# Performance work log

Measured on AMD Instinct MI355X. Metric: run time of the kernel, lower is better.

Reference implementation:

```python
import math
import jax, jax.numpy as jnp
import numpy as np

B, T, G, E, H, L = 8, 32, 32, 768, 12, 4
S = T * G
HD = E // H


def setup_inputs() -> dict:
    key = jax.random.key(0)
    ks = jax.random.split(key, 10)
    def n(k, shape, s=0.02):
        return s * jax.random.normal(k, shape, jnp.float32)
    return dict(
        x=jax.random.normal(ks[0], (B, T, G, E), jnp.float32),
        study_date=jnp.sort(jax.random.randint(ks[1], (B, T), 0, 50), axis=-1),
        wpe=n(ks[2], (50, E)),
        ln1_w=jnp.ones((L, E)), ln1_b=jnp.zeros((L, E)),
        in_w=n(ks[3], (L, 3 * E, E)), in_b=jnp.zeros((L, 3 * E)),
        out_w=n(ks[4], (L, E, E)), out_b=jnp.zeros((L, E)),
        ln2_w=jnp.ones((L, E)), ln2_b=jnp.zeros((L, E)),
        fc_w=n(ks[5], (L, 4 * E, E)), fc_b=jnp.zeros((L, 4 * E)),
        proj_w=n(ks[6], (L, E, 4 * E), 0.02 / math.sqrt(2 * L)),
        proj_b=jnp.zeros((L, E)),
        lnf_w=jnp.ones((E,)), lnf_b=jnp.zeros((E,)),
    )


def _ln(x, w, b):
    m = x.mean(-1, keepdims=True)
    v = ((x - m) ** 2).mean(-1, keepdims=True)
    return (x - m) / jnp.sqrt(v + 1e-5) * w + b


def _gelu_new(x):
    # NewGELU: 0.5*x*(1+tanh(sqrt(2/pi)*(x+0.044715*x^3)))
    c = np.sqrt(2.0 / np.pi).astype(np.float32)
    return 0.5 * x * (1.0 + jnp.tanh(c * (x + 0.044715 * x ** 3)))


def _mask_bias():
    # block-causal mask: tril over T blocks, each expanded to G x G
    allowed = jnp.tril(jnp.ones((T, T), bool))
    allowed = jnp.repeat(jnp.repeat(allowed, G, axis=0), G, axis=1)  # [S,S]
    return jnp.where(allowed, 0.0, -jnp.inf).astype(jnp.float32)


def reference(x, study_date, wpe, ln1_w, ln1_b, in_w, in_b, out_w, out_b,
              ln2_w, ln2_b, fc_w, fc_b, proj_w, proj_b, lnf_w, lnf_b):
    b, t, g, d = x.shape
    s = t * g
    pos = wpe[jnp.clip(study_date, 0, 49)]  # [B,T,E]
    pos = jnp.broadcast_to(pos[:, :, None, :], (b, t, g, d)).reshape(b, s, d)
    h = x.reshape(b, s, d) + pos
    bias = _mask_bias()  # [S,S]
    inv_sqrt_hd = 1.0 / np.sqrt(HD).astype(np.float32)
    for l in range(L):
        y = _ln(h, ln1_w[l], ln1_b[l])
        qkv = y @ in_w[l].T + in_b[l]  # [B,S,3E]
        q, k, v = jnp.split(qkv, 3, axis=-1)
        q = q.reshape(b, s, H, HD).transpose(0, 2, 1, 3)
        k = k.reshape(b, s, H, HD).transpose(0, 2, 1, 3)
        v = v.reshape(b, s, H, HD).transpose(0, 2, 1, 3)
        att = jnp.einsum('bhqd,bhkd->bhqk', q, k) * inv_sqrt_hd + bias
        att = jax.nn.softmax(att, axis=-1)
        o = jnp.einsum('bhqk,bhkd->bhqd', att, v)
        o = o.transpose(0, 2, 1, 3).reshape(b, s, d)
        h = h + o @ out_w[l].T + out_b[l]
        y2 = _ln(h, ln2_w[l], ln2_b[l])
        h = h + _gelu_new(y2 @ fc_w[l].T + fc_b[l]) @ proj_w[l].T + proj_b[l]
    return _ln(h, lnf_w, lnf_b)
```

## Files before the change

kernel.cpp:

```cpp
#include <hip/hip_runtime.h>
#include <hip/hip_bf16.h>

typedef __attribute__((ext_vector_type(8))) __bf16 bf16x8;
typedef __attribute__((ext_vector_type(4))) float f32x4;

typedef unsigned short u16;

__device__ __forceinline__ u16 f2bf(float f) {
    unsigned int u = __float_as_uint(f);
    u += 0x7FFFu + ((u >> 16) & 1u);
    return (u16)(u >> 16);
}

__device__ __forceinline__ void g2l16(const void* g, void* l) {
    __builtin_amdgcn_global_load_lds(
        (const __attribute__((address_space(1))) void*)g,
        (__attribute__((address_space(3))) void*)l, 16, 0, 0);
}

#define BB 8
#define SS 1024
#define EE 768
#define HH 12
#define HD 64
#define LL 4

__global__ __launch_bounds__(256) void cvt_k(const float* __restrict__ in,
                                             u16* __restrict__ out, int n4) {
    for (int i = blockIdx.x * 256 + threadIdx.x; i < n4; i += gridDim.x * 256) {
        float4 v = ((const float4*)in)[i];
        ushort4 u;
        u.x = f2bf(v.x); u.y = f2bf(v.y); u.z = f2bf(v.z); u.w = f2bf(v.w);
        ((ushort4*)out)[i] = u;
    }
}

__global__ __launch_bounds__(256) void embed_k(const float* __restrict__ x,
                                               const int* __restrict__ sd,
                                               const float* __restrict__ wpe,
                                               float* __restrict__ h) {
    int idx = blockIdx.x * 256 + threadIdx.x;
    int e4 = idx % 192;
    int bs = idx / 192;
    int b = bs >> 10;
    int t = (bs >> 5) & 31;
    int date = sd[b * 32 + t];
    date = date < 0 ? 0 : (date > 49 ? 49 : date);
    float4 xv = ((const float4*)x)[idx];
    float4 pv = ((const float4*)wpe)[date * 192 + e4];
    float4 r; r.x = xv.x + pv.x; r.y = xv.y + pv.y; r.z = xv.z + pv.z; r.w = xv.w + pv.w;
    ((float4*)h)[idx] = r;
}

template <bool BF16OUT>
__global__ __launch_bounds__(256) void ln_k(const float* __restrict__ in,
                                            const float* __restrict__ w,
                                            const float* __restrict__ b,
                                            void* __restrict__ out) {
    int tid = threadIdx.x, wv = tid >> 6, lane = tid & 63;
    int token = blockIdx.x * 4 + wv;
    const float4* ip = (const float4*)(in + (size_t)token * EE);
    float4 v[3];
#pragma unroll
    for (int p = 0; p < 3; p++) v[p] = ip[p * 64 + lane];
    float s = 0.f;
#pragma unroll
    for (int p = 0; p < 3; p++) s += v[p].x + v[p].y + v[p].z + v[p].w;
#pragma unroll
    for (int m = 1; m < 64; m <<= 1) s += __shfl_xor(s, m);
    float mean = s * (1.f / 768.f);
    float vs = 0.f;
#pragma unroll
    for (int p = 0; p < 3; p++) {
        float dx = v[p].x - mean, dy = v[p].y - mean, dz = v[p].z - mean, dw = v[p].w - mean;
        vs += dx * dx + dy * dy + dz * dz + dw * dw;
    }
#pragma unroll
    for (int m = 1; m < 64; m <<= 1) vs += __shfl_xor(vs, m);
    float rstd = rsqrtf(vs * (1.f / 768.f) + 1e-5f);
    const float4* wp = (const float4*)w;
    const float4* bp = (const float4*)b;
#pragma unroll
    for (int p = 0; p < 3; p++) {
        float4 wv4 = wp[p * 64 + lane], bv4 = bp[p * 64 + lane];
        float rx = (v[p].x - mean) * rstd * wv4.x + bv4.x;
        float ry = (v[p].y - mean) * rstd * wv4.y + bv4.y;
        float rz = (v[p].z - mean) * rstd * wv4.z + bv4.z;
        float rw = (v[p].w - mean) * rstd * wv4.w + bv4.w;
        if (BF16OUT) {
            ushort4 u; u.x = f2bf(rx); u.y = f2bf(ry); u.z = f2bf(rz); u.w = f2bf(rw);
            ((ushort4*)((u16*)out + (size_t)token * EE))[p * 64 + lane] = u;
        } else {
            float4 r; r.x = rx; r.y = ry; r.z = rz; r.w = rw;
            ((float4*)((float*)out + (size_t)token * EE))[p * 64 + lane] = r;
        }
    }
}

template <int MODE, int BM>
__global__ __launch_bounds__(256) void gemm_bt(const u16* __restrict__ A,
                                               const u16* __restrict__ Bw,
                                               const float* __restrict__ bias,
                                               float* __restrict__ hres,
                                               u16* __restrict__ outb,
                                               u16* __restrict__ vT,
                                               u16* __restrict__ kT,
                                               int M, int N, int K) {
    constexpr int TM = BM / 32;
    constexpr int ABUF = BM * 32;
    __shared__ u16 As[2][ABUF];
    __shared__ u16 Bs[2][4096];
    const int tid = threadIdx.x;
    const int lane = tid & 63, w = tid >> 6;
    const int quad = lane >> 4, l16 = lane & 15;

    const int nx = N >> 7;
    const int ny = M / BM;
    const int id = blockIdx.x;
    const int xcd = id & 7, s = id >> 3;
    const int yt = xcd * (ny >> 3) + s / nx;
    const int xt = s % nx;
    const int m0 = yt * BM, n0 = xt * 128;
    const int wm = (w >> 1) * (BM / 2), wn = (w & 1) * 64;

    f32x4 acc[TM][4];
#pragma unroll
    for (int i = 0; i < TM; i++)
#pragma unroll
        for (int j = 0; j < 4; j++) acc[i][j] = (f32x4){0.f, 0.f, 0.f, 0.f};

    const int cB0 = w * 128 + lane, cB1 = cB0 + 64;
    const int rB0 = cB0 >> 2, gB0 = (((cB0 & 3) ^ ((cB0 >> 3) & 3)) * 8);
    const int rB1 = cB1 >> 2, gB1 = (((cB1 & 3) ^ ((cB1 >> 3) & 3)) * 8);
    const u16* Bp0 = Bw + (size_t)(n0 + rB0) * K + gB0;
    const u16* Bp1 = Bw + (size_t)(n0 + rB1) * K + gB1;
    char* lB0 = (char*)Bs + w * 2048;
    char* lB1 = (char*)Bs + w * 2048 + 1024;
    const int cA0 = (BM == 128) ? cB0 : (w * 64 + lane);
    const int rA0 = cA0 >> 2, gA0 = (((cA0 & 3) ^ ((cA0 >> 3) & 3)) * 8);
    const u16* Ap0 = A + (size_t)(m0 + rA0) * K + gA0;
    char* lA0 = (char*)As + ((BM == 128) ? w * 2048 : w * 1024);
    const int cA1 = cB1;
    const int rA1 = cA1 >> 2, gA1 = (((cA1 & 3) ^ ((cA1 >> 3) & 3)) * 8);
    const u16* Ap1 = A + (size_t)(m0 + rA1) * K + gA1;
    char* lA1 = (char*)As + w * 2048 + 1024;

    const int swz = (quad ^ ((l16 >> 1) & 3)) * 8;

    const int nk = K >> 5;
    g2l16(Ap0, lA0);
    if (BM == 128) g2l16(Ap1, lA1);
    g2l16(Bp0, lB0); g2l16(Bp1, lB1);

    for (int ki = 0; ki < nk; ki++) {
        __syncthreads();
        if (ki + 1 < nk) {
            const int kb = (ki + 1) << 5;
            const int boA = ((ki + 1) & 1) * (ABUF * 2);
            const int boB = ((ki + 1) & 1) * 8192;
            g2l16(Ap0 + kb, lA0 + boA);
            if (BM == 128) g2l16(Ap1 + kb, lA1 + boA);
            g2l16(Bp0 + kb, lB0 + boB);
            g2l16(Bp1 + kb, lB1 + boB);
        }
        const u16* Ab = (const u16*)As + (ki & 1) * ABUF;
        const u16* Bb = (const u16*)Bs + (ki & 1) * 4096;
        bf16x8 af[TM], bfr[4];
#pragma unroll
        for (int t = 0; t < TM; t++) {
            int rowA = wm + t * 16 + l16;
            af[t] = *(const bf16x8*)(Ab + rowA * 32 + swz);
        }
#pragma unroll
        for (int t = 0; t < 4; t++) {
            int rowB = wn + t * 16 + l16;
            bfr[t] = *(const bf16x8*)(Bb + rowB * 32 + swz);
        }
#pragma unroll
        for (int tm = 0; tm < TM; tm++)
#pragma unroll
            for (int tn = 0; tn < 4; tn++)
                acc[tm][tn] = __builtin_amdgcn_mfma_f32_16x16x32_bf16(
                    af[tm], bfr[tn], acc[tm][tn], 0, 0, 0);
    }

#pragma unroll
    for (int tm = 0; tm < TM; tm++) {
        int rowm = m0 + wm + tm * 16 + quad * 4;
#pragma unroll
        for (int tn = 0; tn < 4; tn++) {
            int coln = n0 + wn + tn * 16 + l16;
            float bv = bias[coln];
            f32x4 v = acc[tm][tn];
            if (MODE == 0) {
                int b = rowm >> 10, s2 = rowm & 1023;
                if (coln < EE) {
                    int hh = coln >> 6, d = coln & 63;
                    u16* qp = outb + ((size_t)(b * HH + hh) * SS + s2) * HD + d;
#pragma unroll
                    for (int r = 0; r < 4; r++) qp[r * HD] = f2bf(v[r] + bv);
                } else if (coln < 2 * EE) {
                    int hh = (coln - EE) >> 6, d = (coln - EE) & 63;
                    u16* kp = kT + ((size_t)(b * HH + hh) * SS + s2) * HD + d;
#pragma unroll
                    for (int r = 0; r < 4; r++) kp[r * HD] = f2bf(v[r] + bv);
                } else {
                    int hh = (coln - 2 * EE) >> 6, d = (coln - 2 * EE) & 63;
                    ushort4 pk;
                    pk.x = f2bf(v[0] + bv); pk.y = f2bf(v[1] + bv);
                    pk.z = f2bf(v[2] + bv); pk.w = f2bf(v[3] + bv);
                    *(ushort4*)(vT + (((size_t)((b * HH + hh) * HD + d)) << 10) + s2) = pk;
                }
            } else if (MODE == 1) {
#pragma unroll
                for (int r = 0; r < 4; r++) {
                    size_t idx = (size_t)(rowm + r) * N + coln;
                    hres[idx] += v[r] + bv;
                }
            } else {
#pragma unroll
                for (int r = 0; r < 4; r++) {
                    float x = v[r] + bv;
                    float t = x + 0.044715f * x * x * x;
                    float e = __expf(-1.5957691216057308f * t);
                    float th = (1.f - e) / (1.f + e);
                    outb[(size_t)(rowm + r) * N + coln] = f2bf(0.5f * x * (1.f + th));
                }
            }
        }
    }
}

__global__ __launch_bounds__(256) void attn_k(const u16* __restrict__ qT,
                                              const u16* __restrict__ kT,
                                              const u16* __restrict__ vT,
                                              u16* __restrict__ o) {
    __shared__ u16 Ks[2048];
    __shared__ u16 Vs[2048];
    __shared__ u16 P[4][16 * 40];
    int tid = threadIdx.x, w = tid >> 6, lane = tid & 63;
    int quad = lane >> 4, l16 = lane & 15;
    int blk = blockIdx.x;
    int qg = 15 - (blk / 96);
    int bh = blk % 96;
    int b = bh / HH, hh = bh % HH;
    int q0 = qg * 64;
    int kend_blk = q0 + 64;
    int kend_w = q0 + ((w >> 1) ? 64 : 32);

    const u16* qbase = qT + ((size_t)bh * SS + q0 + w * 16 + l16) * HD + quad * 8;
    bf16x8 qf0 = *(const bf16x8*)(qbase);
    bf16x8 qf1 = *(const bf16x8*)(qbase + 32);

    f32x4 of[4];
#pragma unroll
    for (int i = 0; i < 4; i++) of[i] = (f32x4){0.f, 0.f, 0.f, 0.f};
    float mrun[4], lrun[4];
#pragma unroll
    for (int r = 0; r < 4; r++) { mrun[r] = -__builtin_inff(); lrun[r] = 0.f; }

    int tK = tid >> 3, dcK = ((tid & 7) ^ (tK & 7));
    const u16* kg = kT + ((size_t)bh * SS + tK) * HD + dcK * 8;
    char* kl = (char*)Ks + w * 1024;
    int dV = tid >> 2, tcV = ((tid & 3) ^ ((dV >> 1) & 3));
    const u16* vg = vT + ((size_t)bh * HD + dV) * SS + tcV * 8;
    char* vl = (char*)Vs + w * 1024;
    u16* Pw = P[w];

    for (int kb = 0; kb < kend_blk; kb += 32) {
        g2l16(kg + (size_t)kb * HD, kl);
        g2l16(vg + kb, vl);
        __syncthreads();
        if (kb < kend_w) {
            int t0 = l16, t1 = 16 + l16;
            bf16x8 k00 = *(const bf16x8*)(Ks + (t0 * 8 + (quad ^ (l16 & 7))) * 8);
            bf16x8 k01 = *(const bf16x8*)(Ks + (t0 * 8 + ((4 + quad) ^ (l16 & 7))) * 8);
            bf16x8 k10 = *(const bf16x8*)(Ks + (t1 * 8 + (quad ^ (l16 & 7))) * 8);
            bf16x8 k11 = *(const bf16x8*)(Ks + (t1 * 8 + ((4 + quad) ^ (l16 & 7))) * 8);
            f32x4 s0 = (f32x4){0.f, 0.f, 0.f, 0.f};
            f32x4 s1 = (f32x4){0.f, 0.f, 0.f, 0.f};
            s0 = __builtin_amdgcn_mfma_f32_16x16x32_bf16(qf0, k00, s0, 0, 0, 0);
            s0 = __builtin_amdgcn_mfma_f32_16x16x32_bf16(qf1, k01, s0, 0, 0, 0);
            s1 = __builtin_amdgcn_mfma_f32_16x16x32_bf16(qf0, k10, s1, 0, 0, 0);
            s1 = __builtin_amdgcn_mfma_f32_16x16x32_bf16(qf1, k11, s1, 0, 0, 0);

            float alpha[4];
#pragma unroll
            for (int r = 0; r < 4; r++) {
                float a0 = s0[r] * 0.125f, a1 = s1[r] * 0.125f;
                float mx = fmaxf(a0, a1);
#pragma unroll
                for (int m = 1; m < 16; m <<= 1) mx = fmaxf(mx, __shfl_xor(mx, m));
                float mnew = fmaxf(mrun[r], mx);
                alpha[r] = __expf(mrun[r] - mnew);
                float p0 = __expf(a0 - mnew);
                float p1 = __expf(a1 - mnew);
                float ps = p0 + p1;
#pragma unroll
                for (int m = 1; m < 16; m <<= 1) ps += __shfl_xor(ps, m);
                lrun[r] = lrun[r] * alpha[r] + ps;
                mrun[r] = mnew;
                Pw[(quad * 4 + r) * 40 + l16] = f2bf(p0);
                Pw[(quad * 4 + r) * 40 + 16 + l16] = f2bf(p1);
            }
#pragma unroll
            for (int n4 = 0; n4 < 4; n4++) {
                of[n4][0] *= alpha[0]; of[n4][1] *= alpha[1];
                of[n4][2] *= alpha[2]; of[n4][3] *= alpha[3];
            }
            bf16x8 pf = *(const bf16x8*)(Pw + l16 * 40 + quad * 8);
#pragma unroll
            for (int n4 = 0; n4 < 4; n4++) {
                int d = n4 * 16 + l16;
                bf16x8 vf = *(const bf16x8*)(Vs + (d * 4 + (quad ^ ((d >> 1) & 3))) * 8);
                of[n4] = __builtin_amdgcn_mfma_f32_16x16x32_bf16(pf, vf, of[n4], 0, 0, 0);
            }
        }
        __syncthreads();
    }

    float inv[4];
#pragma unroll
    for (int r = 0; r < 4; r++) inv[r] = 1.f / lrun[r];
#pragma unroll
    for (int n4 = 0; n4 < 4; n4++)
#pragma unroll
        for (int r = 0; r < 4; r++)
            o[(size_t)(b * SS + q0 + w * 16 + quad * 4 + r) * EE + hh * HD + n4 * 16 + l16] =
                f2bf(of[n4][r] * inv[r]);
}

extern "C" void kernel_launch(void* const* d_in, const int* in_sizes, int n_in,
                              void* d_out, int out_size, void* d_ws, size_t ws_size,
                              hipStream_t stream) {
    const float* x     = (const float*)d_in[0];
    const int*   sd    = (const int*)d_in[1];
    const float* wpe   = (const float*)d_in[2];
    const float* ln1w  = (const float*)d_in[3];
    const float* ln1b  = (const float*)d_in[4];
    const float* in_w  = (const float*)d_in[5];
    const float* in_b  = (const float*)d_in[6];
    const float* out_w = (const float*)d_in[7];
    const float* out_b = (const float*)d_in[8];
    const float* ln2w  = (const float*)d_in[9];
    const float* ln2b  = (const float*)d_in[10];
    const float* fc_w  = (const float*)d_in[11];
    const float* fc_b  = (const float*)d_in[12];
    const float* pr_w  = (const float*)d_in[13];
    const float* pr_b  = (const float*)d_in[14];
    const float* lnfw  = (const float*)d_in[15];
    const float* lnfb  = (const float*)d_in[16];
    float* outp = (float*)d_out;

    char* ws = (char*)d_ws;
    float* h   = (float*)ws;
    u16* ybuf  = (u16*)(ws + 25165824);
    u16* big   = (u16*)(ws + 37748736);
    u16* qT    = big;
    u16* kT    = big + 6291456;
    u16* vT    = (u16*)(ws + 88080384);
    u16* wb    = (u16*)(ws + 100663296);
    u16* w_in  = wb;
    u16* w_out = w_in + 7077888;
    u16* w_fc  = w_out + 2359296;
    u16* w_pr  = w_fc + 9437184;

    cvt_k<<<1024, 256, 0, stream>>>(in_w,  w_in,  7077888 / 4);
    cvt_k<<<1024, 256, 0, stream>>>(out_w, w_out, 2359296 / 4);
    cvt_k<<<1024, 256, 0, stream>>>(fc_w,  w_fc,  9437184 / 4);
    cvt_k<<<1024, 256, 0, stream>>>(pr_w,  w_pr,  9437184 / 4);
    embed_k<<<6144, 256, 0, stream>>>(x, sd, wpe, h);

    for (int l = 0; l < LL; l++) {
        ln_k<true><<<2048, 256, 0, stream>>>(h, ln1w + l * EE, ln1b + l * EE, ybuf);
        gemm_bt<0, 128><<<18 * 64, 256, 0, stream>>>(
            ybuf, w_in + (size_t)l * 2304 * 768, in_b + l * 2304, nullptr, qT, vT, kT,
            8192, 2304, 768);
        attn_k<<<1536, 256, 0, stream>>>(qT, kT, vT, ybuf);
        gemm_bt<1, 64><<<6 * 128, 256, 0, stream>>>(
            ybuf, w_out + (size_t)l * 768 * 768, out_b + l * 768, h, nullptr, nullptr, nullptr,
            8192, 768, 768);
        ln_k<true><<<2048, 256, 0, stream>>>(h, ln2w + l * EE, ln2b + l * EE, ybuf);
        gemm_bt<2, 128><<<24 * 64, 256, 0, stream>>>(
            ybuf, w_fc + (size_t)l * 3072 * 768, fc_b + l * 3072, nullptr, big, nullptr, nullptr,
            8192, 3072, 768);
        gemm_bt<1, 64><<<6 * 128, 256, 0, stream>>>(
            big, w_pr + (size_t)l * 768 * 3072, pr_b + l * 768, h, nullptr, nullptr, nullptr,
            8192, 768, 3072);
    }
    ln_k<false><<<2048, 256, 0, stream>>>(h, lnfw, lnfb, outp);
}
```

Measured before the change: 1.343 ms.

## Use 4-stage LDS ring with prefetch distance 2 for BM=64 GEMM

For the BM=64 GEMM variant, the double-buffered LDS staging is replaced with a four-slot ring buffer that prefetches two K-steps ahead. Explicit vmcnt waits plus a bare s_barrier stand in for __syncthreads, so loads stay in flight across iterations. The BM=128 path is left functionally unchanged. This trades more LDS per block (48KB) for deeper latency hiding, which may reduce occupancy, and it depends on hand-coded waitcnt encodings being correct.

Result: no change. 1.332 ms (-0.9%).

```diff
diff --git a/kernel.cpp b/kernel.cpp
--- a/kernel.cpp
+++ b/kernel.cpp
@@ -107,9 +107,6 @@
                                                u16* __restrict__ kT,
                                                int M, int N, int K) {
     constexpr int TM = BM / 32;
-    constexpr int ABUF = BM * 32;
-    __shared__ u16 As[2][ABUF];
-    __shared__ u16 Bs[2][4096];
     const int tid = threadIdx.x;
     const int lane = tid & 63, w = tid >> 6;
     const int quad = lane >> 4, l16 = lane & 15;
@@ -129,59 +126,102 @@
 #pragma unroll
         for (int j = 0; j < 4; j++) acc[i][j] = (f32x4){0.f, 0.f, 0.f, 0.f};
 
-    const int cB0 = w * 128 + lane, cB1 = cB0 + 64;
-    const int rB0 = cB0 >> 2, gB0 = (((cB0 & 3) ^ ((cB0 >> 3) & 3)) * 8);
-    const int rB1 = cB1 >> 2, gB1 = (((cB1 & 3) ^ ((cB1 >> 3) & 3)) * 8);
-    const u16* Bp0 = Bw + (size_t)(n0 + rB0) * K + gB0;
-    const u16* Bp1 = Bw + (size_t)(n0 + rB1) * K + gB1;
-    char* lB0 = (char*)Bs + w * 2048;
-    char* lB1 = (char*)Bs + w * 2048 + 1024;
-    const int cA0 = (BM == 128) ? cB0 : (w * 64 + lane);
-    const int rA0 = cA0 >> 2, gA0 = (((cA0 & 3) ^ ((cA0 >> 3) & 3)) * 8);
-    const u16* Ap0 = A + (size_t)(m0 + rA0) * K + gA0;
-    char* lA0 = (char*)As + ((BM == 128) ? w * 2048 : w * 1024);
-    const int cA1 = cB1;
-    const int rA1 = cA1 >> 2, gA1 = (((cA1 & 3) ^ ((cA1 >> 3) & 3)) * 8);
-    const u16* Ap1 = A + (size_t)(m0 + rA1) * K + gA1;
-    char* lA1 = (char*)As + w * 2048 + 1024;
-
     const int swz = (quad ^ ((l16 >> 1) & 3)) * 8;
-
     const int nk = K >> 5;
-    g2l16(Ap0, lA0);
-    if (BM == 128) g2l16(Ap1, lA1);
-    g2l16(Bp0, lB0); g2l16(Bp1, lB1);
-
-    for (int ki = 0; ki < nk; ki++) {
-        __syncthreads();
-        if (ki + 1 < nk) {
-            const int kb = (ki + 1) << 5;
-            const int boA = ((ki + 1) & 1) * (ABUF * 2);
-            const int boB = ((ki + 1) & 1) * 8192;
-            g2l16(Ap0 + kb, lA0 + boA);
-            if (BM == 128) g2l16(Ap1 + kb, lA1 + boA);
-            g2l16(Bp0 + kb, lB0 + boB);
-            g2l16(Bp1 + kb, lB1 + boB);
+
+    if constexpr (BM == 128) {
+        __shared__ u16 As[2][4096];
+        __shared__ u16 Bs[2][4096];
+        const int c0 = w * 128 + lane, c1 = c0 + 64;
+        const int r0 = c0 >> 2, g0 = (((c0 & 3) ^ ((c0 >> 3) & 3)) * 8);
+        const int r1 = c1 >> 2, g1 = (((c1 & 3) ^ ((c1 >> 3) & 3)) * 8);
+        const u16* Ap0 = A + (size_t)(m0 + r0) * K + g0;
+        const u16* Ap1 = A + (size_t)(m0 + r1) * K + g1;
+        const u16* Bp0 = Bw + (size_t)(n0 + r0) * K + g0;
+        const u16* Bp1 = Bw + (size_t)(n0 + r1) * K + g1;
+        char* lA0 = (char*)As + w * 2048;
+        char* lA1 = (char*)As + w * 2048 + 1024;
+        char* lB0 = (char*)Bs + w * 2048;
+        char* lB1 = (char*)Bs + w * 2048 + 1024;
+
+        g2l16(Ap0, lA0); g2l16(Ap1, lA1); g2l16(Bp0, lB0); g2l16(Bp1, lB1);
+
+        for (int ki = 0; ki < nk; ki++) {
+            __syncthreads();
+            if (ki + 1 < nk) {
+                const int kb = (ki + 1) << 5;
+                const int bo = ((ki + 1) & 1) * 8192;
+                g2l16(Ap0 + kb, lA0 + bo);
+                g2l16(Ap1 + kb, lA1 + bo);
+                g2l16(Bp0 + kb, lB0 + bo);
+                g2l16(Bp1 + kb, lB1 + bo);
+            }
+            const u16* Ab = (const u16*)As + (ki & 1) * 4096;
+            const u16* Bb = (const u16*)Bs + (ki & 1) * 4096;
+            bf16x8 af[TM], bfr[4];
+#pragma unroll
+            for (int t = 0; t < TM; t++)
+                af[t] = *(const bf16x8*)(Ab + (wm + t * 16 + l16) * 32 + swz);
+#pragma unroll
+            for (int t = 0; t < 4; t++)
+                bfr[t] = *(const bf16x8*)(Bb + (wn + t * 16 + l16) * 32 + swz);
+#pragma unroll
+            for (int tm = 0; tm < TM; tm++)
+#pragma unroll
+                for (int tn = 0; tn < 4; tn++)
+                    acc[tm][tn] = __builtin_amdgcn_mfma_f32_16x16x32_bf16(
+                        af[tm], bfr[tn], acc[tm][tn], 0, 0, 0);
         }
-        const u16* Ab = (const u16*)As + (ki & 1) * ABUF;
-        const u16* Bb = (const u16*)Bs + (ki & 1) * 4096;
-        bf16x8 af[TM], bfr[4];
-#pragma unroll
-        for (int t = 0; t < TM; t++) {
-            int rowA = wm + t * 16 + l16;
-            af[t] = *(const bf16x8*)(Ab + rowA * 32 + swz);
+    } else {
+        __shared__ u16 SM[4 * 6144];
+        const int cA = tid;
+        const int rA = cA >> 2, gA = (((cA & 3) ^ ((cA >> 3) & 3)) * 8);
+        const u16* Ap = A + (size_t)(m0 + rA) * K + gA;
+        const int cB0 = w * 128 + lane, cB1 = cB0 + 64;
+        const int rB0 = cB0 >> 2, gB0 = (((cB0 & 3) ^ ((cB0 >> 3) & 3)) * 8);
+        const int rB1 = cB1 >> 2, gB1 = (((cB1 & 3) ^ ((cB1 >> 3) & 3)) * 8);
+        const u16* Bp0 = Bw + (size_t)(n0 + rB0) * K + gB0;
+        const u16* Bp1 = Bw + (size_t)(n0 + rB1) * K + gB1;
+        char* lA = (char*)SM + w * 1024;
+        char* lB0 = (char*)SM + 4096 + w * 2048;
+        char* lB1 = (char*)SM + 4096 + w * 2048 + 1024;
+
+        g2l16(Ap, lA);
+        g2l16(Bp0, lB0);
+        g2l16(Bp1, lB1);
+        g2l16(Ap + 32, lA + 12288);
+        g2l16(Bp0 + 32, lB0 + 12288);
+        g2l16(Bp1 + 32, lB1 + 12288);
+
+        for (int ki = 0; ki < nk; ki++) {
+            if (ki + 2 < nk) {
+                const int kb = (ki + 2) << 5;
+                const int bo = ((ki + 2) & 3) * 12288;
+                g2l16(Ap + kb, lA + bo);
+                g2l16(Bp0 + kb, lB0 + bo);
+                g2l16(Bp1 + kb, lB1 + bo);
+            }
+            if (ki < nk - 2)       __builtin_amdgcn_s_waitcnt(0x0F76);
+            else if (ki == nk - 2) __builtin_amdgcn_s_waitcnt(0x0F73);
+            else                   __builtin_amdgcn_s_waitcnt(0x0F70);
+            __builtin_amdgcn_s_barrier();
+
+            const u16* Ab = (const u16*)SM + (ki & 3) * 6144;
+            const u16* Bb = Ab + 2048;
+            bf16x8 af[TM], bfr[4];
+#pragma unroll
+            for (int t = 0; t < TM; t++)
+                af[t] = *(const bf16x8*)(Ab + (wm + t * 16 + l16) * 32 + swz);
+#pragma unroll
+            for (int t = 0; t < 4; t++)
+                bfr[t] = *(const bf16x8*)(Bb + (wn + t * 16 + l16) * 32 + swz);
+#pragma unroll
+            for (int tm = 0; tm < TM; tm++)
+#pragma unroll
+                for (int tn = 0; tn < 4; tn++)
+                    acc[tm][tn] = __builtin_amdgcn_mfma_f32_16x16x32_bf16(
+                        af[tm], bfr[tn], acc[tm][tn], 0, 0, 0);
         }
-#pragma unroll
-        for (int t = 0; t < 4; t++) {
-            int rowB = wn + t * 16 + l16;
-            bfr[t] = *(const bf16x8*)(Bb + rowB * 32 + swz);
-        }
-#pragma unroll
-        for (int tm = 0; tm < TM; tm++)
-#pragma unroll
-            for (int tn = 0; tn < 4; tn++)
-                acc[tm][tn] = __builtin_amdgcn_mfma_f32_16x16x32_bf16(
-                    af[tm], bfr[tn], acc[tm][tn], 0, 0, 0);
     }
 
 #pragma unroll
```

## Deepen GEMM global-to-LDS pipeline with multi-stage ring buffer and vmcnt waits

Applied to the files above, without the earlier changes.

Replaces the double-buffered LDS tiles in the bf16 GEMM with a 3- or 4-stage ring buffer that prefetches one or two K-tiles ahead. Explicit s_waitcnt vmcnt values plus a raw s_barrier replace the per-iteration __syncthreads. The aim is to hide global load latency better and cut synchronisation overhead. The cost is more LDS per block, which may lower occupancy, and a dependence on hand-computed waitcnt encodings.

New measurement: 1.302 ms. -3.1%, faster.

```diff
diff --git a/kernel.cpp b/kernel.cpp
--- a/kernel.cpp
+++ b/kernel.cpp
@@ -107,9 +107,13 @@
                                                u16* __restrict__ kT,
                                                int M, int N, int K) {
     constexpr int TM = BM / 32;
-    constexpr int ABUF = BM * 32;
-    __shared__ u16 As[2][ABUF];
-    __shared__ u16 Bs[2][4096];
+    constexpr int NST = (BM == 128) ? 3 : 4;
+    constexpr int PD = NST - 2;
+    constexpr int ATILE = BM * 32;
+    constexpr int TILE = ATILE + 4096;
+    constexpr int SSTR = TILE * 2;
+    __shared__ u16 SM[NST * TILE];
+
     const int tid = threadIdx.x;
     const int lane = tid & 63, w = tid >> 6;
     const int quad = lane >> 4, l16 = lane & 15;
@@ -129,59 +133,73 @@
 #pragma unroll
         for (int j = 0; j < 4; j++) acc[i][j] = (f32x4){0.f, 0.f, 0.f, 0.f};
 
+    const int swz = (quad ^ ((l16 >> 1) & 3)) * 8;
+    const int nk = K >> 5;
+
     const int cB0 = w * 128 + lane, cB1 = cB0 + 64;
     const int rB0 = cB0 >> 2, gB0 = (((cB0 & 3) ^ ((cB0 >> 3) & 3)) * 8);
     const int rB1 = cB1 >> 2, gB1 = (((cB1 & 3) ^ ((cB1 >> 3) & 3)) * 8);
     const u16* Bp0 = Bw + (size_t)(n0 + rB0) * K + gB0;
     const u16* Bp1 = Bw + (size_t)(n0 + rB1) * K + gB1;
-    char* lB0 = (char*)Bs + w * 2048;
-    char* lB1 = (char*)Bs + w * 2048 + 1024;
-    const int cA0 = (BM == 128) ? cB0 : (w * 64 + lane);
+    char* lB0 = (char*)SM + ATILE * 2 + w * 2048;
+    char* lB1 = lB0 + 1024;
+    const int cA0 = (BM == 128) ? cB0 : tid;
     const int rA0 = cA0 >> 2, gA0 = (((cA0 & 3) ^ ((cA0 >> 3) & 3)) * 8);
     const u16* Ap0 = A + (size_t)(m0 + rA0) * K + gA0;
-    char* lA0 = (char*)As + ((BM == 128) ? w * 2048 : w * 1024);
+    char* lA0 = (char*)SM + ((BM == 128) ? w * 2048 : w * 1024);
     const int cA1 = cB1;
     const int rA1 = cA1 >> 2, gA1 = (((cA1 & 3) ^ ((cA1 >> 3) & 3)) * 8);
     const u16* Ap1 = A + (size_t)(m0 + rA1) * K + gA1;
-    char* lA1 = (char*)As + w * 2048 + 1024;
-
-    const int swz = (quad ^ ((l16 >> 1) & 3)) * 8;
-
-    const int nk = K >> 5;
+    char* lA1 = (char*)SM + w * 2048 + 1024;
+
     g2l16(Ap0, lA0);
     if (BM == 128) g2l16(Ap1, lA1);
-    g2l16(Bp0, lB0); g2l16(Bp1, lB1);
-
+    g2l16(Bp0, lB0);
+    g2l16(Bp1, lB1);
+    if (PD == 2) {
+        g2l16(Ap0 + 32, lA0 + SSTR);
+        if (BM == 128) g2l16(Ap1 + 32, lA1 + SSTR);
+        g2l16(Bp0 + 32, lB0 + SSTR);
+        g2l16(Bp1 + 32, lB1 + SSTR);
+    }
+
+    int rb = 0, wb = PD;
     for (int ki = 0; ki < nk; ki++) {
-        __syncthreads();
-        if (ki + 1 < nk) {
-            const int kb = (ki + 1) << 5;
-            const int boA = ((ki + 1) & 1) * (ABUF * 2);
-            const int boB = ((ki + 1) & 1) * 8192;
-            g2l16(Ap0 + kb, lA0 + boA);
-            if (BM == 128) g2l16(Ap1 + kb, lA1 + boA);
-            g2l16(Bp0 + kb, lB0 + boB);
-            g2l16(Bp1 + kb, lB1 + boB);
+        if (ki + PD < nk) {
+            const int kb = (ki + PD) << 5;
+            const int bo = wb * SSTR;
+            g2l16(Ap0 + kb, lA0 + bo);
+            if (BM == 128) g2l16(Ap1 + kb, lA1 + bo);
+            g2l16(Bp0 + kb, lB0 + bo);
+            g2l16(Bp1 + kb, lB1 + bo);
         }
-        const u16* Ab = (const u16*)As + (ki & 1) * ABUF;
-        const u16* Bb = (const u16*)Bs + (ki & 1) * 4096;
+        if (BM == 128) {
+            if (ki < nk - 1) __builtin_amdgcn_s_waitcnt(0x0F74);
+            else             __builtin_amdgcn_s_waitcnt(0x0F70);
+        } else {
+            if (ki < nk - 2)      __builtin_amdgcn_s_waitcnt(0x0F76);
+            else if (ki == nk - 2) __builtin_amdgcn_s_waitcnt(0x0F73);
+            else                  __builtin_amdgcn_s_waitcnt(0x0F70);
+        }
+        __builtin_amdgcn_s_barrier();
+
+        const u16* Ab = (const u16*)SM + rb * TILE;
+        const u16* Bb = Ab + ATILE;
         bf16x8 af[TM], bfr[4];
 #pragma unroll
-        for (int t = 0; t < TM; t++) {
-            int rowA = wm + t * 16 + l16;
-            af[t] = *(const bf16x8*)(Ab + rowA * 32 + swz);
-        }
-#pragma unroll
-        for (int t = 0; t < 4; t++) {
-            int rowB = wn + t * 16 + l16;
-            bfr[t] = *(const bf16x8*)(Bb + rowB * 32 + swz);
-        }
+        for (int t = 0; t < TM; t++)
+            af[t] = *(const bf16x8*)(Ab + (wm + t * 16 + l16) * 32 + swz);
+#pragma unroll
+        for (int t = 0; t < 4; t++)
+            bfr[t] = *(const bf16x8*)(Bb + (wn + t * 16 + l16) * 32 + swz);
 #pragma unroll
         for (int tm = 0; tm < TM; tm++)
 #pragma unroll
             for (int tn = 0; tn < 4; tn++)
                 acc[tm][tn] = __builtin_amdgcn_mfma_f32_16x16x32_bf16(
                     af[tm], bfr[tn], acc[tm][tn], 0, 0, 0);
+        rb = (rb + 1 == NST) ? 0 : rb + 1;
+        wb = (wb + 1 == NST) ? 0 : wb + 1;
     }
 
 #pragma unroll
```
